# Optimization experiments

Hardware: AMD Instinct MI355X
Metric: run time of the kernel (lower is better)

The kernel has to match this reference:

```python
import jax, jax.numpy as jnp
import numpy as np
from jax import lax

HS, WS = 8, 8  # pattern_size


def setup_inputs() -> dict:
    key = jax.random.key(0)
    k1, k2, k3 = jax.random.split(key, 3)
    B, C, T, H, W = 2, 64, 16, 112, 112
    Cout, K = 64, 3
    x = jax.random.normal(k1, (B, C, T, H, W), dtype=jnp.float32)
    # one independent Conv3d weight/bias per (h, w) phase in the 8x8 pattern
    weight = jax.random.normal(k2, (HS, WS, Cout, C, K, K, K), dtype=jnp.float32) * 0.05
    bias = jax.random.normal(k3, (HS, WS, Cout), dtype=jnp.float32) * 0.05
    return {"x": x, "weight": weight, "bias": bias}


def reference(x, weight, bias):
    hs, ws = HS, WS
    B, C, T, H, W = x.shape
    Cout = weight.shape[2]
    # torch F.pad(x, (hs-1, hs-1, ws-1, ws-1, 1, 1)): W padded by hs-1, H by ws-1, T by 1
    paded = jnp.pad(x, ((0, 0), (0, 0), (1, 1), (ws - 1, ws - 1), (hs - 1, hs - 1)))
    Ho, Wo = H // hs, W // ws  # conv output spatial size per phase: (H-3)//8 + 1 = H//8
    rows = []
    for h in range(hs):
        cols = []
        for w in range(ws):
            sl = paded[:, :, :, h:H + h, w:W + w]  # [B, C, T+2, H, W]
            y = lax.conv_general_dilated(
                sl, weight[h, w],
                window_strides=(1, hs, ws), padding='VALID',
                dimension_numbers=('NCDHW', 'OIDHW', 'NCDHW'))  # [B, Cout, T, Ho, Wo]
            cols.append(y + bias[h, w][None, :, None, None, None])
        rows.append(jnp.stack(cols, 0))
    res = jnp.stack(rows, 0)  # [hs, ws, B, Cout, T, Ho, Wo]
    # out[:, :, :, h + hs*i, w + ws*j] = res[h, w, :, :, :, i, j]
    out = jnp.transpose(res, (2, 3, 4, 5, 0, 6, 1))  # [B, Cout, T, Ho, hs, Wo, ws]
    return out.reshape(B, Cout, T, H, W)
```

## Files before the change

kernel.cpp:

```cpp
#include <hip/hip_runtime.h>
#include <hip/hip_bf16.h>
#include <stdint.h>

typedef __attribute__((ext_vector_type(8))) short short8;
typedef __attribute__((ext_vector_type(4))) float f32x4;

#define XPP_BYTES 66355200ull
#define XPP_SLACK 65536ull
#define WPP_BYTES 14155776ull

__device__ __forceinline__ void gl2lds16(const void* g, void* l) {
    __builtin_amdgcn_global_load_lds(
        (const __attribute__((address_space(1))) unsigned int*)g,
        (__attribute__((address_space(3))) unsigned int*)l, 16, 0, 0);
}

__global__ __launch_bounds__(256)
void bzero(uint4* __restrict__ xpp) {
    const uint4 z = {0u, 0u, 0u, 0u};
    const int total = 935936;
    for (int idx = blockIdx.x * 256 + threadIdx.x; idx < total;
         idx += gridDim.x * 256) {
        int u;
        if (idx < 276480) {
            int slab = idx / 2160, off = idx % 2160;
            u = slab * 32400 + off;
        } else if (idx < 534528) {
            int k = idx - 276480;
            int run = k / 144, off = k % 144;
            int slab = run / 14, rho = run % 14 + 1;
            u = slab * 32400 + rho * 2160 + off;
        } else {
            int k = idx - 534528;
            int run = k / 8, off = k % 8;
            int slab = run / 392, r2 = run % 392;
            int rho = r2 / 28 + 1, r3 = r2 % 28;
            int cwo = r3 / 2 + 1, d = (r3 & 1) * 17;
            u = slab * 32400 + rho * 2160 + cwo * 144 + d * 8 + off;
        }
        xpp[u] = z;
    }
}

__global__ __launch_bounds__(512)
void xform_x(const float* __restrict__ xin, __hip_bfloat16* __restrict__ xpp) {
    extern __shared__ __hip_bfloat16 Xl[];
    const int bid = blockIdx.x;
    const int rho = bid % 14, d = (bid / 14) % 16, b = bid / 224;
    const int tid = threadIdx.x;
    for (int f = tid; f < 64 * 8 * 28; f += 512) {
        int ci = f / 224, rem = f % 224;
        int r = rem / 28, c4 = (rem % 28) * 4;
        const float4 v = *(const float4*)&xin[
            ((((size_t)b * 64 + ci) * 16 + d) * 112 + (rho * 8 + r)) * 112 + c4];
        const float vv[4] = {v.x, v.y, v.z, v.w};
#pragma unroll
        for (int u = 0; u < 4; ++u) {
            int c = c4 + u;
            Xl[(r * 112 + c) * 64 + (ci ^ ((c & 7) << 3))] = __float2bfloat16(vv[u]);
        }
    }
    __syncthreads();
    for (int f = tid; f < 896 * 8; f += 512) {
        int pos = f >> 3, j = f & 7;
        int r = pos / 112, c = pos % 112;
        int cw = c & 7, cwo = c >> 3;
        uint4 v = *(const uint4*)&Xl[pos * 64 + ((j * 8) ^ ((c & 7) << 3))];
        size_t dst = (((((size_t)(r * 8 + cw) * 2 + b) * 15 + (rho + 1)) * 15
                       + (cwo + 1)) * 18 + (d + 1)) * 64 + j * 8;
        *(uint4*)(xpp + dst) = v;
    }
}

__global__ __launch_bounds__(256)
void xform_w(const float* __restrict__ wt, __hip_bfloat16* __restrict__ wpp) {
    __shared__ __hip_bfloat16 lw[8 * 27 * 72];
    const int hw = blockIdx.x >> 3, cc = blockIdx.x & 7;
    for (int f = threadIdx.x; f < 8 * 64 * 27; f += 256) {
        int k = f % 27, ci = (f / 27) % 64, co = f / (27 * 64);
        float v = wt[(size_t)hw * 110592 + (size_t)(cc * 8 + co) * 1728 + ci * 27 + k];
        lw[(co * 27 + k) * 72 + ci] = __float2bfloat16(v);
    }
    __syncthreads();
    for (int f = threadIdx.x; f < 27 * 8 * 8; f += 256) {
        int cic = f % 8, co = (f / 8) % 8, k = f / 64;
        uint4 v = *(const uint4*)&lw[(co * 27 + k) * 72 + cic * 8];
        size_t dst = (((size_t)hw * 27 + k) * 64 + (cc * 8 + co)) * 64 + cic * 8;
        *(uint4*)(wpp + dst) = v;
    }
}


#define STG(S) do {                                                          \
    const int s3_ = (S);                                                     \
    const int rr_ = s3_ >> 1, kh_ = rr_ / 3, kw_ = rr_ % 3;                  \
    const int r0_ = h + kh_ - 7, c0_ = w + kw_ - 7;                          \
    const char* ap_ = (const char*)xpp +                                     \
        (size_t)(((((r0_ & 7) * 8 + (c0_ & 7)) * 2 + b) * 15                 \
                  + ((r0_ >> 3) + 1 + mc)) * 15 + ((c0_ >> 3) + 1)) * 2304   \
        + (s3_ & 1) * 64;                                                    \
    char* Ad_ = smem + (s3_ & 3) * 16384;                                    \
    _Pragma("unroll")                                                        \
    for (int i_ = 0; i_ < 2; ++i_)                                           \
        gl2lds16(ap_ + srcoff[i_], Ad_ + (uint32_t)(tid + i_ * 512) * 16);   \
} while (0)

#define LDB(S, DST) do {                                                     \
    const int sb_ = (S);                                                     \
    const char* bp_ = wbase + (size_t)(sb_ >> 1) * 8192 + (sb_ & 1) * 64;    \
    _Pragma("unroll")                                                        \
    for (int kd_ = 0; kd_ < 3; ++kd_)                                        \
        DST[kd_] = *(const short8*)(bp_ + kd_ * 73728 + ng * 2048 + bofs);   \
} while (0)

#define WINDOW(S, CUR, NXT, DOB, DOA, WAITN) do {                            \
    if ((WAITN) == 0)      asm volatile("s_waitcnt vmcnt(0)" ::: "memory");  \
    else if ((WAITN) == 4) asm volatile("s_waitcnt vmcnt(4)" ::: "memory");  \
    else                   asm volatile("s_waitcnt vmcnt(2)" ::: "memory");  \
    __builtin_amdgcn_s_barrier();                                            \
    {   const char* Ab_ = smem + ((S) & 3) * 16384;                          \
        _Pragma("unroll")                                                    \
        for (int kd = 0; kd < 3; ++kd) {                                     \
            short8 af_[7];                                                   \
            _Pragma("unroll")                                                \
            for (int j_ = 0; j_ < 7; ++j_)                                   \
                af_[j_] = *(const short8*)(Ab_ + (mg * 7 + j_) * 1152        \
                                           + rofs[kd]);                      \
            if (kd == 0) {                                                   \
                __builtin_amdgcn_sched_barrier(0);                           \
                if (DOB) LDB((S) + 1, NXT);                                  \
                __builtin_amdgcn_sched_barrier(0);                           \
                if (DOA) STG((S) + 3);                                       \
                __builtin_amdgcn_sched_barrier(0);                           \
            }                                                                \
            __builtin_amdgcn_s_setprio(1);                                   \
            _Pragma("unroll")                                                \
            for (int j_ = 0; j_ < 7; ++j_)                                   \
                acc[j_] = __builtin_amdgcn_mfma_f32_16x16x32_bf16(           \
                    af_[j_], CUR[kd], acc[j_], 0, 0, 0);                     \
            __builtin_amdgcn_s_setprio(0);                                   \
        } }                                                                  \
} while (0)

__global__ __launch_bounds__(512, 4)
void patgemm(const __hip_bfloat16* __restrict__ xpp,
             const __hip_bfloat16* __restrict__ wpp,
             const float* __restrict__ bs,
             float* __restrict__ out) {
    extern __shared__ char smem[];
    const int bid = blockIdx.x;
    const int h = bid & 7, k = bid >> 3;
    const int w = k & 7, b = (k >> 3) & 1, mc = k >> 4;
    const int hw = h * 8 + w;
    const int tid = threadIdx.x, wv = tid >> 6, lane = tid & 63;
    const int col = lane & 15, quad = lane >> 4;
    const int mg = wv >> 2, ng = wv & 3;

    uint32_t srcoff[2];
#pragma unroll
    for (int i = 0; i < 2; ++i) {
        int u = tid + i * 512; if (u > 1007) u = 1007;
        int wo = u / 72, rem = u % 72;
        int d = rem >> 2, qp = rem & 3, q = qp ^ ((d >> 1) & 3);
        srcoff[i] = (uint32_t)(wo * 2304 + d * 128 + q * 16);
    }
    uint32_t rofs[3];
#pragma unroll
    for (int kd = 0; kd < 3; ++kd)
        rofs[kd] = (uint32_t)((col + kd) * 64
            + ((quad ^ (((col + kd) >> 1) & 3)) << 4));
    const uint32_t bofs = (uint32_t)(col * 128 + quad * 16);

    f32x4 acc[7];
#pragma unroll
    for (int j = 0; j < 7; ++j) acc[j] = (f32x4){0.f, 0.f, 0.f, 0.f};

    const char* wbase = (const char*)wpp + (size_t)hw * 27 * 8192;
    short8 bfrA[3], bfrB[3];

    STG(0);
    __builtin_amdgcn_sched_barrier(0);
    LDB(0, bfrA);
    __builtin_amdgcn_sched_barrier(0);
    STG(1);
    STG(2);

    WINDOW(0, bfrA, bfrB, 1, 1, 4);
#pragma unroll 1
    for (int kp = 0; kp < 7; ++kp) {
        const int s1 = 2 * kp + 1;
        WINDOW(s1,     bfrB, bfrA, 1, 1, 2);
        WINDOW(s1 + 1, bfrA, bfrB, 1, 1, 2);
    }
    WINDOW(15, bfrB, bfrA, 1, 0, 2);
    WINDOW(16, bfrA, bfrB, 1, 0, 0);
    WINDOW(17, bfrB, bfrA, 0, 0, 0);

    const float* bsl = bs + hw * 64;
    const int y = 8 * mc + h;
    const int co = ng * 16 + col;
    const float bv = bsl[co];
#pragma unroll
    for (int j = 0; j < 7; ++j) {
        const int wo = mg * 7 + j;
        const int x = 8 * wo + w;
#pragma unroll
        for (int jj = 0; jj < 4; ++jj) {
            const int t = quad * 4 + jj;
            out[((((size_t)b * 64 + co) * 16 + t) * 112 + y) * 112 + x]
                = acc[j][jj] + bv;
        }
    }
}

#define XL_ROWSTRIDE 116
#define WL_WSTRIDE (17*27)

__global__ __launch_bounds__(256, 3)
void patconv3d_fp32(const float* __restrict__ xin,
                    const float* __restrict__ wt,
                    const float* __restrict__ bs,
                    float* __restrict__ out) {
    __shared__ float Xl[3*3*7*XL_ROWSTRIDE];
    __shared__ float Wl[8*WL_WSTRIDE];
    const int bid = blockIdx.x;
    const int ct = bid & 3, hb = (bid >> 2) & 1, h = (bid >> 3) & 7;
    const int t = (bid >> 6) & 15, b = (bid >> 10) & 1;
    const int tid = threadIdx.x;
    const int xl = tid & 127, cg = tid >> 7;
    const int xr = (xl < 112) ? xl : 111;
    const int wq = xl & 7;
    float acc[8][7];
#pragma unroll
    for (int c = 0; c < 8; ++c)
#pragma unroll
        for (int ho = 0; ho < 7; ++ho) acc[c][ho] = 0.f;
    for (int ci = 0; ci < 64; ++ci) {
        __syncthreads();
        for (int idx = tid; idx < 3 * 3 * 7 * 114; idx += 256) {
            int c = idx % 114, rest = idx / 114;
            int ho = rest % 7; rest /= 7;
            int kh = rest % 3, kd = rest / 3;
            int r = 8 * (hb * 7 + ho) + h + kh - 7;
            int d = t + kd - 1, colx = c - 7;
            float v = 0.f;
            if (r >= 0 && d >= 0 && d < 16 && colx >= 0)
                v = xin[(((size_t)(b * 64 + ci) * 16 + d) * 112 + r) * 112 + colx];
            Xl[((kd * 3 + kh) * 7 + ho) * XL_ROWSTRIDE + c] = v;
        }
        for (int idx = tid; idx < 8 * 16 * 27; idx += 256) {
            int k2 = idx % 27, rest = idx / 27;
            int co_l = rest % 16, wi = rest / 16;
            Wl[wi * WL_WSTRIDE + co_l * 27 + k2] =
                wt[(((size_t)(h * 8 + wi) * 64 + (ct * 16 + co_l)) * 64 + ci) * 27 + k2];
        }
        __syncthreads();
#pragma unroll
        for (int kd = 0; kd < 3; ++kd)
#pragma unroll
            for (int kh = 0; kh < 3; ++kh)
#pragma unroll
                for (int kw = 0; kw < 3; ++kw) {
                    const int k2 = (kd * 3 + kh) * 3 + kw;
                    float xv[7];
#pragma unroll
                    for (int ho = 0; ho < 7; ++ho)
                        xv[ho] = Xl[((kd * 3 + kh) * 7 + ho) * XL_ROWSTRIDE + xr + kw];
                    float wv[8];
#pragma unroll
                    for (int c = 0; c < 8; ++c)
                        wv[c] = Wl[wq * WL_WSTRIDE + (cg * 8 + c) * 27 + k2];
#pragma unroll
                    for (int c = 0; c < 8; ++c)
#pragma unroll
                        for (int ho = 0; ho < 7; ++ho)
                            acc[c][ho] += wv[c] * xv[ho];
                }
    }
    if (xl < 112) {
#pragma unroll
        for (int c = 0; c < 8; ++c) {
            const int co = ct * 16 + cg * 8 + c;
            const float bv = bs[(h * 8 + wq) * 64 + co];
#pragma unroll
            for (int ho = 0; ho < 7; ++ho) {
                const int y = 8 * (hb * 7 + ho) + h;
                out[(((size_t)(b * 64 + co) * 16 + t) * 112 + y) * 112 + xl] = acc[c][ho] + bv;
            }
        }
    }
}

extern "C" void kernel_launch(void* const* d_in, const int* in_sizes, int n_in,
                              void* d_out, int out_size, void* d_ws, size_t ws_size,
                              hipStream_t stream) {
    const float* x  = (const float*)d_in[0];
    const float* wg = (const float*)d_in[1];
    const float* bi = (const float*)d_in[2];
    float* out = (float*)d_out;
    if (ws_size >= XPP_BYTES + XPP_SLACK + WPP_BYTES) {
        __hip_bfloat16* xpp = (__hip_bfloat16*)d_ws;
        __hip_bfloat16* wpp = (__hip_bfloat16*)((char*)d_ws + XPP_BYTES + XPP_SLACK);
        bzero<<<1024, 256, 0, stream>>>((uint4*)d_ws);
        xform_x<<<448, 512, 114688, stream>>>(x, xpp);
        xform_w<<<512, 256, 0, stream>>>(wg, wpp);
        patgemm<<<1792, 512, 65536, stream>>>(xpp, wpp, bi, out);
    } else {
        patconv3d_fp32<<<2048, 256, 0, stream>>>(x, wg, bi, out);
    }
}
```

Before: 298.0 us.

## Restructure patgemm tiling: 7 waves with 2x4 MFMA tiles and LDS-staged weights

Rewrites the main implicit-GEMM kernel to use 448 threads (7 waves). Each wave now computes a 2x4 grid of 16x16 MFMA tiles, replacing the previous 7x1 strip per wave. Weight fragments are staged through LDS with async global-to-LDS loads and a swizzled layout, instead of being loaded directly into registers. The K loop is reorganized into 27 taps with half-K windows and triple-buffered A/B stages. The workspace is reordered so weights sit first, with the slack padding removed. This targets more operand reuse per LDS read and fewer per-wave global loads, at the cost of more barriers per K step and lower occupancy (3 blocks per CU).

```diff
diff --git a/kernel.cpp b/kernel.cpp
--- a/kernel.cpp
+++ b/kernel.cpp
@@ -5,9 +5,8 @@
 typedef __attribute__((ext_vector_type(8))) short short8;
 typedef __attribute__((ext_vector_type(4))) float f32x4;
 
+#define WPP_BYTES 14155776ull
 #define XPP_BYTES 66355200ull
-#define XPP_SLACK 65536ull
-#define WPP_BYTES 14155776ull
 
 __device__ __forceinline__ void gl2lds16(const void* g, void* l) {
     __builtin_amdgcn_global_load_lds(
@@ -91,124 +90,132 @@
 }
 
 
-#define STG(S) do {                                                          \
-    const int s3_ = (S);                                                     \
-    const int rr_ = s3_ >> 1, kh_ = rr_ / 3, kw_ = rr_ % 3;                  \
-    const int r0_ = h + kh_ - 7, c0_ = w + kw_ - 7;                          \
-    const char* ap_ = (const char*)xpp +                                     \
+#define WAITVM_(N) asm volatile("s_waitcnt vmcnt(" #N ")" ::: "memory")
+#define WAITVM(N) WAITVM_(N)
+
+#define STGA(T, RN, HFA) do {                                                \
+    const int t_ = (T), kd_ = t_ / 9, r9_ = t_ % 9;                          \
+    const int r0_ = h + (r9_ / 3) - 7, c0_ = w + (r9_ % 3) - 7;              \
+    const char* ap_ = xppc +                                                 \
         (size_t)(((((r0_ & 7) * 8 + (c0_ & 7)) * 2 + b) * 15                 \
                   + ((r0_ >> 3) + 1 + mc)) * 15 + ((c0_ >> 3) + 1)) * 2304   \
-        + (s3_ & 1) * 64;                                                    \
-    char* Ad_ = smem + (s3_ & 3) * 16384;                                    \
-    _Pragma("unroll")                                                        \
-    for (int i_ = 0; i_ < 2; ++i_)                                           \
-        gl2lds16(ap_ + srcoff[i_], Ad_ + (uint32_t)(tid + i_ * 512) * 16);   \
+        + kd_ * 128 + (HFA) * 64;                                            \
+    char* Ad_ = smem + (RN) * 14336;                                         \
+    gl2lds16(ap_ + aoff[0], Ad_ + tid * 16);                                 \
+    gl2lds16(ap_ + aoff[1], Ad_ + 7168 + tid * 16);                          \
 } while (0)
 
-#define LDB(S, DST) do {                                                     \
-    const int sb_ = (S);                                                     \
-    const char* bp_ = wbase + (size_t)(sb_ >> 1) * 8192 + (sb_ & 1) * 64;    \
-    _Pragma("unroll")                                                        \
-    for (int kd_ = 0; kd_ < 3; ++kd_)                                        \
-        DST[kd_] = *(const short8*)(bp_ + kd_ * 73728 + ng * 2048 + bofs);   \
+#define STGB(T, RN) do {                                                     \
+    const char* bp_ = wppc + (size_t)hw * 221184 + (size_t)(T) * 8192;       \
+    char* Bd_ = smem + 43008 + (RN) * 8192;                                  \
+    gl2lds16(bp_ + boff[0], Bd_ + tid * 16);                                 \
+    char* d1_ = (wv == 0) ? (Bd_ + 7168 + (tid & 63) * 16)                   \
+                          : (smem + 67584 + (tid & 63) * 16);                \
+    gl2lds16(bp_ + boff[1], d1_);                                            \
 } while (0)
 
-#define WINDOW(S, CUR, NXT, DOB, DOA, WAITN) do {                            \
-    if ((WAITN) == 0)      asm volatile("s_waitcnt vmcnt(0)" ::: "memory");  \
-    else if ((WAITN) == 4) asm volatile("s_waitcnt vmcnt(4)" ::: "memory");  \
-    else                   asm volatile("s_waitcnt vmcnt(2)" ::: "memory");  \
+#define MF(mi, n, AF, BF) acc[mi][n] =                                       \
+    __builtin_amdgcn_mfma_f32_16x16x32_bf16(AF, BF, acc[mi][n], 0, 0, 0)
+
+#define WIN(RA, HF, RB, DOB, TB, RBN, DOA, TA, RAN, HFA, WN) do {            \
+    WAITVM(WN);                                                              \
     __builtin_amdgcn_s_barrier();                                            \
-    {   const char* Ab_ = smem + ((S) & 3) * 16384;                          \
-        _Pragma("unroll")                                                    \
-        for (int kd = 0; kd < 3; ++kd) {                                     \
-            short8 af_[7];                                                   \
-            _Pragma("unroll")                                                \
-            for (int j_ = 0; j_ < 7; ++j_)                                   \
-                af_[j_] = *(const short8*)(Ab_ + (mg * 7 + j_) * 1152        \
-                                           + rofs[kd]);                      \
-            if (kd == 0) {                                                   \
-                __builtin_amdgcn_sched_barrier(0);                           \
-                if (DOB) LDB((S) + 1, NXT);                                  \
-                __builtin_amdgcn_sched_barrier(0);                           \
-                if (DOA) STG((S) + 3);                                       \
-                __builtin_amdgcn_sched_barrier(0);                           \
-            }                                                                \
-            __builtin_amdgcn_s_setprio(1);                                   \
-            _Pragma("unroll")                                                \
-            for (int j_ = 0; j_ < 7; ++j_)                                   \
-                acc[j_] = __builtin_amdgcn_mfma_f32_16x16x32_bf16(           \
-                    af_[j_], CUR[kd], acc[j_], 0, 0, 0);                     \
-            __builtin_amdgcn_s_setprio(0);                                   \
-        } }                                                                  \
+    const char* Ab_ = smem + (RA) * 14336;                                   \
+    const char* Bb_ = smem + 43008 + (RB) * 8192;                            \
+    short8 af0 = *(const short8*)(Ab_ + wv * 2048 + arow);                   \
+    short8 af1 = *(const short8*)(Ab_ + wv * 2048 + 1024 + arow);            \
+    short8 bf0 = *(const short8*)(Bb_ + bofsw[HF]);                          \
+    short8 bf1 = *(const short8*)(Bb_ + 2048 + bofsw[HF]);                   \
+    short8 bf2 = *(const short8*)(Bb_ + 4096 + bofsw[HF]);                   \
+    short8 bf3 = *(const short8*)(Bb_ + 6144 + bofsw[HF]);                   \
+    __builtin_amdgcn_sched_barrier(0);                                       \
+    if (DOB) STGB(TB, RBN);                                                  \
+    if (DOA) STGA(TA, RAN, HFA);                                             \
+    __builtin_amdgcn_sched_barrier(0);                                       \
+    __builtin_amdgcn_s_setprio(1);                                           \
+    MF(0, 0, af0, bf0); MF(0, 1, af0, bf1);                                  \
+    MF(0, 2, af0, bf2); MF(0, 3, af0, bf3);                                  \
+    MF(1, 0, af1, bf0); MF(1, 1, af1, bf1);                                  \
+    MF(1, 2, af1, bf2); MF(1, 3, af1, bf3);                                  \
+    __builtin_amdgcn_s_setprio(0);                                           \
 } while (0)
 
-__global__ __launch_bounds__(512, 4)
+__global__ __launch_bounds__(448, 3)
 void patgemm(const __hip_bfloat16* __restrict__ xpp,
-             const __hip_bfloat16* __restrict__ wpp,
+             const char* __restrict__ wppc,
              const float* __restrict__ bs,
              float* __restrict__ out) {
     extern __shared__ char smem[];
+    const char* xppc = (const char*)xpp;
     const int bid = blockIdx.x;
     const int h = bid & 7, k = bid >> 3;
     const int w = k & 7, b = (k >> 3) & 1, mc = k >> 4;
     const int hw = h * 8 + w;
-    const int tid = threadIdx.x, wv = tid >> 6, lane = tid & 63;
-    const int col = lane & 15, quad = lane >> 4;
-    const int mg = wv >> 2, ng = wv & 3;
-
-    uint32_t srcoff[2];
+    const int tid = threadIdx.x, wv = tid >> 6;
+    const int lane = tid & 63, col = lane & 15, quad = lane >> 4;
+
+    uint32_t aoff[2];
 #pragma unroll
     for (int i = 0; i < 2; ++i) {
-        int u = tid + i * 512; if (u > 1007) u = 1007;
-        int wo = u / 72, rem = u % 72;
-        int d = rem >> 2, qp = rem & 3, q = qp ^ ((d >> 1) & 3);
-        srcoff[i] = (uint32_t)(wo * 2304 + d * 128 + q * 16);
-    }
-    uint32_t rofs[3];
-#pragma unroll
-    for (int kd = 0; kd < 3; ++kd)
-        rofs[kd] = (uint32_t)((col + kd) * 64
-            + ((quad ^ (((col + kd) >> 1) & 3)) << 4));
-    const uint32_t bofs = (uint32_t)(col * 128 + quad * 16);
-
-    f32x4 acc[7];
-#pragma unroll
-    for (int j = 0; j < 7; ++j) acc[j] = (f32x4){0.f, 0.f, 0.f, 0.f};
-
-    const char* wbase = (const char*)wpp + (size_t)hw * 27 * 8192;
-    short8 bfrA[3], bfrB[3];
-
-    STG(0);
+        int u = tid + i * 448;
+        aoff[i] = (uint32_t)((u >> 6) * 2304 + ((u >> 2) & 15) * 128
+                             + (((u & 3) ^ ((u >> 4) & 3)) << 4));
+    }
+    uint32_t boff[2];
+#pragma unroll
+    for (int i = 0; i < 2; ++i) {
+        int u = tid + i * 448;
+        boff[i] = (uint32_t)((u >> 3) * 128 + (((u & 7) ^ ((u >> 3) & 7)) << 4));
+    }
+    const uint32_t arow = (uint32_t)(col * 64 + ((quad ^ ((col >> 2) & 3)) << 4));
+    uint32_t bofsw[2];
+#pragma unroll
+    for (int hf = 0; hf < 2; ++hf)
+        bofsw[hf] = (uint32_t)(col * 128 + (((hf * 4 + quad) ^ (col & 7)) << 4));
+
+    f32x4 acc[2][4];
+#pragma unroll
+    for (int mi = 0; mi < 2; ++mi)
+#pragma unroll
+        for (int n = 0; n < 4; ++n) acc[mi][n] = (f32x4){0.f, 0.f, 0.f, 0.f};
+
+    STGB(0, 0);
     __builtin_amdgcn_sched_barrier(0);
-    LDB(0, bfrA);
-    __builtin_amdgcn_sched_barrier(0);
-    STG(1);
-    STG(2);
-
-    WINDOW(0, bfrA, bfrB, 1, 1, 4);
+    STGA(0, 0, 0);
+    STGA(0, 1, 1);
+
 #pragma unroll 1
-    for (int kp = 0; kp < 7; ++kp) {
-        const int s1 = 2 * kp + 1;
-        WINDOW(s1,     bfrB, bfrA, 1, 1, 2);
-        WINDOW(s1 + 1, bfrA, bfrB, 1, 1, 2);
-    }
-    WINDOW(15, bfrB, bfrA, 1, 0, 2);
-    WINDOW(16, bfrA, bfrB, 1, 0, 0);
-    WINDOW(17, bfrB, bfrA, 0, 0, 0);
+    for (int g = 0; g < 8; ++g) {
+        const int t1 = 3 * g + 1, t2 = 3 * g + 2, t3 = 3 * g + 3;
+        WIN(0, 0, 0,  1, t1, 1,  1, t1, 2, 0,  2);
+        WIN(1, 1, 0,  0, 0, 0,   1, t1, 0, 1,  4);
+        WIN(2, 0, 1,  1, t2, 2,  1, t2, 1, 0,  2);
+        WIN(0, 1, 1,  0, 0, 0,   1, t2, 2, 1,  4);
+        WIN(1, 0, 2,  1, t3, 0,  1, t3, 0, 0,  2);
+        WIN(2, 1, 2,  0, 0, 0,   1, t3, 1, 1,  4);
+    }
+    WIN(0, 0, 0,  1, 25, 1,  1, 25, 2, 0,  2);
+    WIN(1, 1, 0,  0, 0, 0,   1, 25, 0, 1,  4);
+    WIN(2, 0, 1,  1, 26, 2,  1, 26, 1, 0,  2);
+    WIN(0, 1, 1,  0, 0, 0,   1, 26, 2, 1,  4);
+    WIN(1, 0, 2,  0, 0, 0,   0, 0, 0, 0,   2);
+    WIN(2, 1, 2,  0, 0, 0,   0, 0, 0, 0,   0);
 
     const float* bsl = bs + hw * 64;
     const int y = 8 * mc + h;
-    const int co = ng * 16 + col;
-    const float bv = bsl[co];
-#pragma unroll
-    for (int j = 0; j < 7; ++j) {
-        const int wo = mg * 7 + j;
-        const int x = 8 * wo + w;
-#pragma unroll
-        for (int jj = 0; jj < 4; ++jj) {
-            const int t = quad * 4 + jj;
-            out[((((size_t)b * 64 + co) * 16 + t) * 112 + y) * 112 + x]
-                = acc[j][jj] + bv;
+#pragma unroll
+    for (int mi = 0; mi < 2; ++mi) {
+        const int x = 8 * (2 * wv + mi) + w;
+#pragma unroll
+        for (int n = 0; n < 4; ++n) {
+            const int co = n * 16 + col;
+            const float bv = bsl[co];
+#pragma unroll
+            for (int jj = 0; jj < 4; ++jj) {
+                const int t = quad * 4 + jj;
+                out[((((size_t)b * 64 + co) * 16 + t) * 112 + y) * 112 + x]
+                    = acc[mi][n][jj] + bv;
+            }
         }
     }
 }
@@ -298,13 +305,13 @@
     const float* wg = (const float*)d_in[1];
     const float* bi = (const float*)d_in[2];
     float* out = (float*)d_out;
-    if (ws_size >= XPP_BYTES + XPP_SLACK + WPP_BYTES) {
-        __hip_bfloat16* xpp = (__hip_bfloat16*)d_ws;
-        __hip_bfloat16* wpp = (__hip_bfloat16*)((char*)d_ws + XPP_BYTES + XPP_SLACK);
-        bzero<<<1024, 256, 0, stream>>>((uint4*)d_ws);
+    if (ws_size >= WPP_BYTES + XPP_BYTES) {
+        __hip_bfloat16* wpp = (__hip_bfloat16*)d_ws;
+        __hip_bfloat16* xpp = (__hip_bfloat16*)((char*)d_ws + WPP_BYTES);
+        bzero<<<1024, 256, 0, stream>>>((uint4*)xpp);
         xform_x<<<448, 512, 114688, stream>>>(x, xpp);
         xform_w<<<512, 256, 0, stream>>>(wg, wpp);
-        patgemm<<<1792, 512, 65536, stream>>>(xpp, wpp, bi, out);
+        patgemm<<<1792, 448, 68608, stream>>>(xpp, (const char*)wpp, bi, out);
     } else {
         patconv3d_fp32<<<2048, 256, 0, stream>>>(x, wg, bi, out);
     }
```

After: 298.2 us. No clear change (+0.1%).
